# Kernel tuning notes

Hardware: AMD Instinct MI355X
Metric: run time of the kernel (lower is better)

Reference implementation:

```python
import jax, jax.numpy as jnp
import numpy as np

NY, NX, DIM = 4096, 50000, 3
RADIUS = 1.4
BOX = 14.3  # chosen so ~16 y-neighbors per x point at radius 1.4
LAYERS = [3, 128, 256, 3]  # kernel_in_dim=3 -> hidden [128,256] -> dim=3


def _radius_neighbors(x, y, r):
    """Brute-force radius search: edges (x_index i, nbr_index j) with |x_i - y_j| <= r."""
    r2 = r * r
    xi, yj = [], []
    for s in range(0, x.shape[0], 5000):
        xc = x[s:s + 5000]
        d2 = ((xc[:, None, :] - y[None, :, :]) ** 2).sum(-1)
        ii, jj = np.nonzero(d2 <= r2)
        xi.append(ii + s)
        yj.append(jj)
    return np.concatenate(yj).astype(np.int64), np.concatenate(xi).astype(np.int64)


def setup_inputs() -> dict:
    rng = np.random.default_rng(0)
    y = rng.uniform(0.0, BOX, (NY, DIM)).astype(np.float32)   # rom_ic points
    x = rng.uniform(0.0, BOX, (NX, DIM)).astype(np.float32)   # fom_ic points
    f_y = rng.standard_normal((NY, DIM)).astype(np.float32)   # rom_f values
    nbr_index, x_index = _radius_neighbors(x, y, RADIUS)

    key = jax.random.key(0)
    ks = jax.random.split(key, 3)
    params = {}
    for i in range(3):
        fan_in = LAYERS[i]
        params[f"W{i+1}"] = (jax.random.normal(ks[i], (LAYERS[i], LAYERS[i + 1]), jnp.float32)
                             / np.float32(np.sqrt(fan_in)))
        params[f"b{i+1}"] = jnp.zeros((LAYERS[i + 1],), jnp.float32)

    return dict(rom_ic=jnp.asarray(y)[None], fom_ic=jnp.asarray(x)[None],
                rom_f=jnp.asarray(f_y)[None],
                nbr_index=jnp.asarray(nbr_index), x_index=jnp.asarray(x_index),
                **params)


def _kernel_mlp(h, W1, b1, W2, b2, W3, b3):
    h = jax.nn.gelu(h @ W1 + b1)
    h = jax.nn.gelu(h @ W2 + b2)
    return h @ W3 + b3


def reference(rom_ic, fom_ic, rom_f, W1, b1, W2, b2, W3, b3, nbr_index, x_index):
    y = rom_ic[0]      # [NY,3] source points
    x = fom_ic[0]      # [NX,3] target points
    f_y = rom_f[0]     # [NY,3] source function values

    rel = y[nbr_index] - x[x_index]                    # [E,3] per-edge kernel input
    k = _kernel_mlp(rel, W1, b1, W2, b2, W3, b3)       # [E,3] kernel values
    msg = k * f_y[nbr_index]                           # 'linear' transform: k(x,y) * f(y)

    num = jax.ops.segment_sum(msg, x_index, num_segments=x.shape[0])        # [NX,3]
    cnt = jax.ops.segment_sum(jnp.ones((msg.shape[0],), msg.dtype), x_index,
                              num_segments=x.shape[0])                      # [NX]
    out = num / jnp.maximum(cnt, 1.0)[:, None]         # mean over neighbors (0 if none)
    return out[None]                                    # [1, NX, 3]
```

## Files before the change

kernel.cpp:

```cpp
#include <hip/hip_runtime.h>
#include <hip/hip_bf16.h>

typedef __bf16 bf16x8 __attribute__((ext_vector_type(8)));
typedef float  f32x4  __attribute__((ext_vector_type(4)));
typedef float  f32x2  __attribute__((ext_vector_type(2)));
typedef float  f32x16 __attribute__((ext_vector_type(16)));
typedef int    i32x4  __attribute__((ext_vector_type(4)));

__device__ __forceinline__ f32x2 gelu2(f32x2 x) {
    f32x2 x2 = x * x;
    f32x2 t  = x2 * 0.044715f + 1.0f;
    f32x2 a  = (x * -1.5957691216057308f) * t;
    f32x2 e  = { __expf(a.x), __expf(a.y) };
    f32x2 d  = e + 1.0f;
    f32x2 r  = { __builtin_amdgcn_rcpf(d.x), __builtin_amdgcn_rcpf(d.y) };
    return x * r;
}

__device__ __forceinline__ unsigned int pack2bf(float a, float b) {
    unsigned short ua = __builtin_bit_cast(unsigned short, (__bf16)a);
    unsigned short ub = __builtin_bit_cast(unsigned short, (__bf16)b);
    return (unsigned int)ua | ((unsigned int)ub << 16);
}

__device__ __forceinline__ bf16x8 frag_from_pk(unsigned int q0, unsigned int q1,
                                               unsigned int q2, unsigned int q3) {
    auto p02 = __builtin_amdgcn_permlane32_swap((int)q0, (int)q2, false, false);
    auto p13 = __builtin_amdgcn_permlane32_swap((int)q1, (int)q3, false, false);
    i32x4 fri = { static_cast<int>(p02[0]), static_cast<int>(p13[0]),
                  static_cast<int>(p02[1]), static_cast<int>(p13[1]) };
    return __builtin_bit_cast(bf16x8, fri);
}

__global__ void prep_weights(const float* __restrict__ W2, const float* __restrict__ W3,
                             const float* __restrict__ W1,
                             __bf16* __restrict__ w2t, __bf16* __restrict__ w3t,
                             __bf16* __restrict__ w1tp) {
    int idx = blockIdx.x * 256 + threadIdx.x;
    if (idx < 32768) {
        int k = idx >> 8;
        int u = idx & 255;
        w2t[u * 128 + k] = (__bf16)W2[idx];
    } else if (idx < 32768 + 8192) {
        int t = idx - 32768;
        int d = t >> 8;
        int u = t & 255;
        w3t[t] = (__bf16)(d < 3 ? W3[u * 3 + d] : 0.0f);
    } else if (idx < 32768 + 8192 + 2048) {
        int t = idx - 40960;
        int u = t >> 4;
        int k = t & 15;
        w1tp[t] = (k < 3) ? (__bf16)W1[k * 128 + u] : (__bf16)0.0f;
    }
}

__launch_bounds__(512, 4)
__global__ void edge_mlp(const float* __restrict__ y, const float* __restrict__ x,
                         const float* __restrict__ fy,
                         const int* __restrict__ nbr, const int* __restrict__ xidx,
                         const __bf16* __restrict__ w1tp, const float* __restrict__ b1,
                         const __bf16* __restrict__ w2t, const float* __restrict__ b2,
                         const __bf16* __restrict__ w3t, const float* __restrict__ b3,
                         float* __restrict__ out, int E) {
    __shared__ __attribute__((aligned(16))) __bf16 w2l[256 * 128];
    __shared__ float msgS[8][32][3];
    __shared__ int   isS[8][32];

    const int tid  = threadIdx.x;
    const int wid  = tid >> 6;
    const int lane = tid & 63;
    const int l31  = lane & 31;
    const int b    = lane >> 5;

    {
        int u = tid >> 1, half = tid & 1;
        const __bf16* src = w2t + u * 128 + half * 64;
        char* rowbase = (char*)w2l + u * 256;
        int sw = (u & 15) << 4;
        #pragma unroll
        for (int j = 0; j < 8; ++j) {
            bf16x8 v = *(const bf16x8*)(src + j * 8);
            *(bf16x8*)(rowbase + ((half * 128 + j * 16) ^ sw)) = v;
        }
    }

    const int g = blockIdx.x * 256 + wid * 32 + l31;
    int   iidx = -1;
    float fy0 = 0.0f, fy1 = 0.0f, fy2 = 0.0f;
    bf16x8 rv = { (__bf16)0.0f, (__bf16)0.0f, (__bf16)0.0f, (__bf16)0.0f,
                  (__bf16)0.0f, (__bf16)0.0f, (__bf16)0.0f, (__bf16)0.0f };
    if (b == 0 && g < E) {
        int j = nbr[g];
        iidx  = xidx[g];
        rv[0] = (__bf16)(y[j*3+0] - x[iidx*3+0]);
        rv[1] = (__bf16)(y[j*3+1] - x[iidx*3+1]);
        rv[2] = (__bf16)(y[j*3+2] - x[iidx*3+2]);
        fy0 = fy[j*3+0];
        fy1 = fy[j*3+1];
        fy2 = fy[j*3+2];
    }
    const bf16x8 relB = rv;

    bf16x8 B2[8];
    #pragma unroll
    for (int ut1 = 0; ut1 < 4; ++ut1) {
        f32x16 c;
        #pragma unroll
        for (int q = 0; q < 16; ++q) c[q] = 0.0f;
        bf16x8 a1 = *(const bf16x8*)&w1tp[(ut1 * 32 + l31) * 16 + b * 8];
        c = __builtin_amdgcn_mfma_f32_32x32x16_bf16(a1, relB, c, 0, 0, 0);

        int u0 = ut1 * 32 + 4 * b;
        f32x4 b1q[4];
        #pragma unroll
        for (int gq = 0; gq < 4; ++gq)
            b1q[gq] = *(const f32x4*)(b1 + u0 + 8 * gq);

        unsigned int pw[8];
        #pragma unroll
        for (int gq = 0; gq < 4; ++gq) {
            f32x2 s01 = { c[4*gq+0] + b1q[gq][0], c[4*gq+1] + b1q[gq][1] };
            f32x2 s23 = { c[4*gq+2] + b1q[gq][2], c[4*gq+3] + b1q[gq][3] };
            f32x2 g01 = gelu2(s01);
            f32x2 g23 = gelu2(s23);
            pw[2*gq+0] = pack2bf(g01.x, g01.y);
            pw[2*gq+1] = pack2bf(g23.x, g23.y);
        }
        B2[2*ut1+0] = frag_from_pk(pw[0], pw[1], pw[2], pw[3]);
        B2[2*ut1+1] = frag_from_pk(pw[4], pw[5], pw[6], pw[7]);
    }
    __syncthreads();

    f32x16 acc3;
    #pragma unroll
    for (int q = 0; q < 16; ++q) acc3[q] = 0.0f;

    #pragma unroll
    for (int ut = 0; ut < 8; ++ut) {
        f32x16 c;
        #pragma unroll
        for (int q = 0; q < 16; ++q) c[q] = 0.0f;
        {
            const int u = ut * 32 + l31;
            const char* rowbase = (const char*)w2l + u * 256;
            const int sw = (u & 15) << 4;
            #pragma unroll
            for (int kt = 0; kt < 8; ++kt) {
                bf16x8 a2 = *(const bf16x8*)(rowbase + ((kt * 32 + b * 16) ^ sw));
                c = __builtin_amdgcn_mfma_f32_32x32x16_bf16(a2, B2[kt], c, 0, 0, 0);
            }
        }

        int u0 = ut * 32 + 4 * b;
        f32x4 b2q[4];
        #pragma unroll
        for (int gq = 0; gq < 4; ++gq)
            b2q[gq] = *(const f32x4*)(b2 + u0 + 8 * gq);

        unsigned int pw[8];
        #pragma unroll
        for (int gq = 0; gq < 4; ++gq) {
            f32x2 s01 = { c[4*gq+0] + b2q[gq][0], c[4*gq+1] + b2q[gq][1] };
            f32x2 s23 = { c[4*gq+2] + b2q[gq][2], c[4*gq+3] + b2q[gq][3] };
            f32x2 g01 = gelu2(s01);
            f32x2 g23 = gelu2(s23);
            pw[2*gq+0] = pack2bf(g01.x, g01.y);
            pw[2*gq+1] = pack2bf(g23.x, g23.y);
        }

        #pragma unroll
        for (int ki = 0; ki < 2; ++ki) {
            bf16x8 bfr = frag_from_pk(pw[4*ki+0], pw[4*ki+1], pw[4*ki+2], pw[4*ki+3]);
            bf16x8 a3  = *(const bf16x8*)&w3t[l31 * 256 + ut * 32 + ki * 16 + b * 8];
            acc3 = __builtin_amdgcn_mfma_f32_32x32x16_bf16(a3, bfr, acc3, 0, 0, 0);
        }
    }

    if (b == 0) {
        float m0 = 0.0f, m1 = 0.0f, m2 = 0.0f;
        if (iidx >= 0) {
            m0 = (acc3[0] + b3[0]) * fy0;
            m1 = (acc3[1] + b3[1]) * fy1;
            m2 = (acc3[2] + b3[2]) * fy2;
        }
        msgS[wid][l31][0] = m0;
        msgS[wid][l31][1] = m1;
        msgS[wid][l31][2] = m2;
        isS[wid][l31] = iidx;
        bool leader = (iidx >= 0) && (l31 == 0 || isS[wid][l31 - 1] != iidx);
        if (leader) {
            float s0 = 0.0f, s1 = 0.0f, s2 = 0.0f;
            int j = l31;
            while (j < 32 && isS[wid][j] == iidx) {
                s0 += msgS[wid][j][0];
                s1 += msgS[wid][j][1];
                s2 += msgS[wid][j][2];
                ++j;
            }
            unsafeAtomicAdd(&out[iidx*3+0], s0);
            unsafeAtomicAdd(&out[iidx*3+1], s1);
            unsafeAtomicAdd(&out[iidx*3+2], s2);
        }
    }
}

__global__ void finalize_div(float* __restrict__ out, const int* __restrict__ xidx,
                             int E, int nx) {
    int i = blockIdx.x * blockDim.x + threadIdx.x;
    if (i >= nx) return;
    int lo = 0, hi = E;
    while (lo < hi) { int mid = (lo + hi) >> 1; if (xidx[mid] < i) lo = mid + 1; else hi = mid; }
    int start = lo;
    hi = E;
    while (lo < hi) { int mid = (lo + hi) >> 1; if (xidx[mid] < i + 1) lo = mid + 1; else hi = mid; }
    int cnt = lo - start;
    float inv = 1.0f / (float)(cnt > 1 ? cnt : 1);
    out[i*3+0] *= inv;
    out[i*3+1] *= inv;
    out[i*3+2] *= inv;
}

extern "C" void kernel_launch(void* const* d_in, const int* in_sizes, int n_in,
                              void* d_out, int out_size, void* d_ws, size_t ws_size,
                              hipStream_t stream) {
    const float* y   = (const float*)d_in[0];
    const float* x   = (const float*)d_in[1];
    const float* fyp = (const float*)d_in[2];
    const int*   nbr = (const int*)d_in[3];
    const int*   xix = (const int*)d_in[4];
    const float* W1  = (const float*)d_in[5];
    const float* b1  = (const float*)d_in[6];
    const float* W2  = (const float*)d_in[7];
    const float* b2  = (const float*)d_in[8];
    const float* W3  = (const float*)d_in[9];
    const float* b3  = (const float*)d_in[10];
    float* out = (float*)d_out;

    int E  = in_sizes[3];
    int nx = in_sizes[1] / 3;
    __bf16* w2t  = (__bf16*)d_ws;
    __bf16* w3t  = (__bf16*)((char*)d_ws + 65536);
    __bf16* w1tp = (__bf16*)((char*)d_ws + 81920);

    hipMemsetAsync(d_out, 0, (size_t)out_size * sizeof(float), stream);
    prep_weights<<<168, 256, 0, stream>>>(W2, W3, W1, w2t, w3t, w1tp);

    int nblocks = (E + 255) / 256;
    edge_mlp<<<nblocks, 512, 0, stream>>>(y, x, fyp, nbr, xix, w1tp, b1, w2t, b2, w3t, b3, out, E);

    finalize_div<<<(nx + 255) / 256, 256, 0, stream>>>(out, xix, E, nx);
}
```

Baseline: 146.0 us.

## Split hidden-256 layer across two blocks per edge tile to halve LDS

Each edge tile is now processed by two blocks, each handling half of the 256 second-layer hidden units and loading only that half of W2 into shared memory. Layer-3 partial sums from the two halves are combined through the existing atomic adds, with b3 added only by the first half. This halves LDS use per block, which should allow more resident blocks, and spreads the work over twice as many blocks. In exchange, the first layer, the gathers and the edge loads are computed twice, and the atomic traffic to the output doubles.

Result: slower. 182.5 us (+25.0%).

```diff
diff --git a/kernel.cpp b/kernel.cpp
--- a/kernel.cpp
+++ b/kernel.cpp
@@ -62,29 +62,31 @@
                          const __bf16* __restrict__ w2t, const float* __restrict__ b2,
                          const __bf16* __restrict__ w3t, const float* __restrict__ b3,
                          float* __restrict__ out, int E) {
-    __shared__ __attribute__((aligned(16))) __bf16 w2l[256 * 128];
+    __shared__ __attribute__((aligned(16))) __bf16 w2l[128 * 128];
     __shared__ float msgS[8][32][3];
     __shared__ int   isS[8][32];
 
-    const int tid  = threadIdx.x;
-    const int wid  = tid >> 6;
-    const int lane = tid & 63;
-    const int l31  = lane & 31;
-    const int b    = lane >> 5;
+    const int tid   = threadIdx.x;
+    const int wid   = tid >> 6;
+    const int lane  = tid & 63;
+    const int l31   = lane & 31;
+    const int b     = lane >> 5;
+    const int uhalf = blockIdx.x & 1;
+    const int tile  = blockIdx.x >> 1;
 
     {
-        int u = tid >> 1, half = tid & 1;
-        const __bf16* src = w2t + u * 128 + half * 64;
-        char* rowbase = (char*)w2l + u * 256;
-        int sw = (u & 15) << 4;
-        #pragma unroll
-        for (int j = 0; j < 8; ++j) {
+        int ul = tid >> 2, q = tid & 3;
+        const __bf16* src = w2t + (uhalf * 128 + ul) * 128 + q * 32;
+        char* rowbase = (char*)w2l + ul * 256;
+        int sw = (ul & 15) << 4;
+        #pragma unroll
+        for (int j = 0; j < 4; ++j) {
             bf16x8 v = *(const bf16x8*)(src + j * 8);
-            *(bf16x8*)(rowbase + ((half * 128 + j * 16) ^ sw)) = v;
-        }
-    }
-
-    const int g = blockIdx.x * 256 + wid * 32 + l31;
+            *(bf16x8*)(rowbase + ((q * 64 + j * 16) ^ sw)) = v;
+        }
+    }
+
+    const int g = tile * 256 + wid * 32 + l31;
     int   iidx = -1;
     float fy0 = 0.0f, fy1 = 0.0f, fy2 = 0.0f;
     bf16x8 rv = { (__bf16)0.0f, (__bf16)0.0f, (__bf16)0.0f, (__bf16)0.0f,
@@ -136,14 +138,14 @@
     for (int q = 0; q < 16; ++q) acc3[q] = 0.0f;
 
     #pragma unroll
-    for (int ut = 0; ut < 8; ++ut) {
+    for (int ut = 0; ut < 4; ++ut) {
         f32x16 c;
         #pragma unroll
         for (int q = 0; q < 16; ++q) c[q] = 0.0f;
         {
-            const int u = ut * 32 + l31;
-            const char* rowbase = (const char*)w2l + u * 256;
-            const int sw = (u & 15) << 4;
+            const int ul = ut * 32 + l31;
+            const char* rowbase = (const char*)w2l + ul * 256;
+            const int sw = (ul & 15) << 4;
             #pragma unroll
             for (int kt = 0; kt < 8; ++kt) {
                 bf16x8 a2 = *(const bf16x8*)(rowbase + ((kt * 32 + b * 16) ^ sw));
@@ -151,7 +153,7 @@
             }
         }
 
-        int u0 = ut * 32 + 4 * b;
+        int u0 = uhalf * 128 + ut * 32 + 4 * b;
         f32x4 b2q[4];
         #pragma unroll
         for (int gq = 0; gq < 4; ++gq)
@@ -171,7 +173,7 @@
         #pragma unroll
         for (int ki = 0; ki < 2; ++ki) {
             bf16x8 bfr = frag_from_pk(pw[4*ki+0], pw[4*ki+1], pw[4*ki+2], pw[4*ki+3]);
-            bf16x8 a3  = *(const bf16x8*)&w3t[l31 * 256 + ut * 32 + ki * 16 + b * 8];
+            bf16x8 a3  = *(const bf16x8*)&w3t[l31 * 256 + uhalf * 128 + ut * 32 + ki * 16 + b * 8];
             acc3 = __builtin_amdgcn_mfma_f32_32x32x16_bf16(a3, bfr, acc3, 0, 0, 0);
         }
     }
@@ -179,9 +181,12 @@
     if (b == 0) {
         float m0 = 0.0f, m1 = 0.0f, m2 = 0.0f;
         if (iidx >= 0) {
-            m0 = (acc3[0] + b3[0]) * fy0;
-            m1 = (acc3[1] + b3[1]) * fy1;
-            m2 = (acc3[2] + b3[2]) * fy2;
+            float c0 = uhalf ? 0.0f : b3[0];
+            float c1 = uhalf ? 0.0f : b3[1];
+            float c2 = uhalf ? 0.0f : b3[2];
+            m0 = (acc3[0] + c0) * fy0;
+            m1 = (acc3[1] + c1) * fy1;
+            m2 = (acc3[2] + c2) * fy2;
         }
         msgS[wid][l31][0] = m0;
         msgS[wid][l31][1] = m1;
@@ -245,7 +250,7 @@
     hipMemsetAsync(d_out, 0, (size_t)out_size * sizeof(float), stream);
     prep_weights<<<168, 256, 0, stream>>>(W2, W3, W1, w2t, w3t, w1tp);
 
-    int nblocks = (E + 255) / 256;
+    int nblocks = 2 * ((E + 255) / 256);
     edge_mlp<<<nblocks, 512, 0, stream>>>(y, x, fyp, nbr, xix, w1tp, b1, w2t, b2, w3t, b3, out, E);
 
     finalize_div<<<(nx + 255) / 256, 256, 0, stream>>>(out, xix, E, nx);
```
